# Kernel tuning notes

Hardware: AMD Instinct MI355X
Metric: run time of the kernel (lower is better)

## Reference

```python
import jax, jax.numpy as jnp
import numpy as np

VOCAB, D_IN, D_H, D_OUT, B, S = 32000, 512, 1024, 64, 64, 256


def setup_inputs() -> dict:
    key = jax.random.key(0)
    ks = jax.random.split(key, 8)
    s_in = 1.0 / np.sqrt(D_H)
    return {
        "x": jax.random.randint(ks[0], (B, S), 0, VOCAB),
        "emb": jax.random.normal(ks[1], (VOCAB, D_IN), jnp.float32),
        "w_ih": jax.random.uniform(ks[2], (3 * D_H, D_IN), jnp.float32, -s_in, s_in),
        "w_hh": jax.random.uniform(ks[3], (3 * D_H, D_H), jnp.float32, -s_in, s_in),
        "b_ih": jax.random.uniform(ks[4], (3 * D_H,), jnp.float32, -s_in, s_in),
        "b_hh": jax.random.uniform(ks[5], (3 * D_H,), jnp.float32, -s_in, s_in),
        "fc_w": jax.random.uniform(ks[6], (D_OUT, D_H), jnp.float32, -s_in, s_in),
        "fc_b": jax.random.uniform(ks[7], (D_OUT,), jnp.float32, -s_in, s_in),
    }


def _gru_seq(xe, w_ih, w_hh, b_ih, b_hh):
    # xe: [B, S, D_IN] -> hidden states [B, S, D_H]
    h0 = jnp.zeros((xe.shape[0], D_H), xe.dtype)
    # precompute input projections for all timesteps: [S, B, 3H]
    gi_all = jnp.einsum('bsd,gd->sbg', xe, w_ih) + b_ih

    def step(h, gi):
        gh = h @ w_hh.T + b_hh
        gi_r, gi_z, gi_n = jnp.split(gi, 3, axis=-1)
        gh_r, gh_z, gh_n = jnp.split(gh, 3, axis=-1)
        r = jax.nn.sigmoid(gi_r + gh_r)
        z = jax.nn.sigmoid(gi_z + gh_z)
        n = jnp.tanh(gi_n + r * gh_n)
        h_new = (1.0 - z) * n + z * h
        return h_new, h_new

    _, hs = jax.lax.scan(step, h0, gi_all)  # hs: [S, B, H]
    return jnp.transpose(hs, (1, 0, 2))  # [B, S, H]


def reference(x, emb, w_ih, w_hh, b_ih, b_hh, fc_w, fc_b):
    xe = emb[x]  # [B, S, D_IN]
    outs = _gru_seq(xe, w_ih, w_hh, b_ih, b_hh)  # [B, S, H]
    logits = jnp.einsum('bsh,oh->bso', outs, fc_w) + fc_b
    return jax.nn.log_softmax(logits, axis=2)
```

## Files before the change

kernel.cpp:

```cpp
#include <hip/hip_runtime.h>
#include <stdint.h>
#include <math.h>

typedef short short8 __attribute__((ext_vector_type(8)));
typedef float floatx4 __attribute__((ext_vector_type(4)));

#define MFMA(a, b, c) __builtin_amdgcn_mfma_f32_16x16x32_bf16((a), (b), (c), 0, 0, 0)

#define B_   64
#define S_   256
#define DIN  512
#define DH   1024
#define G3   3072
#define DOUT 64
#define M_   (B_ * S_)
#define NBLK 128
#define FPAD 16
#define NFLAG (S_ * 2 * 128 * FPAD)

#define AGENT_LD_U32(p) __hip_atomic_load((p), __ATOMIC_RELAXED, __HIP_MEMORY_SCOPE_AGENT)
#define AGENT_ST_U32(p, v) __hip_atomic_store((p), (v), __ATOMIC_RELAXED, __HIP_MEMORY_SCOPE_AGENT)

typedef __attribute__((address_space(1))) const void* gas_t;
typedef __attribute__((address_space(3))) void* las_t;

__device__ __forceinline__ unsigned short f2bf(float f) {
    union { float f; uint32_t u; } v; v.f = f;
    uint32_t u = v.u;
    uint32_t r = (u + 0x7fffu + ((u >> 16) & 1u)) >> 16;
    return (unsigned short)r;
}
__device__ __forceinline__ float bf2f(unsigned short s) {
    union { uint32_t u; float f; } v; v.u = ((uint32_t)s) << 16; return v.f;
}
__device__ __forceinline__ short8 ld8(const unsigned short* p) {
    return *reinterpret_cast<const short8*>(p);
}
__device__ __forceinline__ float fast_sigmoid(float x) {
    return 1.f / (1.f + __expf(-x));
}
__device__ __forceinline__ float fast_tanh(float x) {
    return 1.f - 2.f / (__expf(2.f * x) + 1.f);
}

__global__ void cast_bf16_kernel(const float* __restrict__ src,
                                 unsigned short* __restrict__ dst, int n) {
    int i = blockIdx.x * 256 + threadIdx.x;
    if (i < n) dst[i] = f2bf(src[i]);
}

__global__ void init_flags_kernel(unsigned int* flags) {
    int i = blockIdx.x * 256 + threadIdx.x;
    if (i < NFLAG) flags[i] = 0u;
}

__global__ void gather_kernel(const int* __restrict__ x, const float* __restrict__ emb,
                              unsigned short* __restrict__ xe) {
    int g = blockIdx.x * 256 + threadIdx.x;
    int m = g >> 9;
    int k = g & 511;
    int s = m >> 6, b = m & 63;
    int tok = x[b * S_ + s];
    xe[(size_t)m * DIN + k] = f2bf(emb[(size_t)tok * DIN + k]);
}

__global__ __launch_bounds__(256) void gemm_bt_bias(
        const unsigned short* __restrict__ A, const unsigned short* __restrict__ W,
        const float* __restrict__ bias, unsigned short* __restrict__ C,
        int M, int N, int K) {
    __shared__ __align__(16) unsigned short As[128 * 32];
    __shared__ __align__(16) unsigned short Ws[128 * 32];
    int tid = threadIdx.x;
    int lane = tid & 63, wv = tid >> 6;
    int wm = wv >> 1, wn = wv & 1;
    int q = lane >> 4, l15 = lane & 15;
    int bm = blockIdx.x, bn = blockIdx.y;

    floatx4 acc[4][4];
    floatx4 z = {0.f, 0.f, 0.f, 0.f};
    for (int i = 0; i < 4; i++) for (int j = 0; j < 4; j++) acc[i][j] = z;

    const int c0 = wv * 2;
    const int rowc = lane >> 2;
    const int colc = (lane & 3) * 8;
    const unsigned short* gA0 = A + (size_t)(bm * 128 + c0 * 16 + rowc) * K + colc;
    const unsigned short* gA1 = gA0 + (size_t)16 * K;
    const unsigned short* gW0 = W + (size_t)(bn * 128 + c0 * 16 + rowc) * K + colc;
    const unsigned short* gW1 = gW0 + (size_t)16 * K;
    unsigned short* lA0 = &As[c0 * 512];
    unsigned short* lA1 = &As[(c0 + 1) * 512];
    unsigned short* lW0 = &Ws[c0 * 512];
    unsigned short* lW1 = &Ws[(c0 + 1) * 512];

    for (int k0 = 0; k0 < K; k0 += 32) {
        __syncthreads();
        __builtin_amdgcn_global_load_lds((gas_t)(gA0 + k0), (las_t)lA0, 16, 0, 0);
        __builtin_amdgcn_global_load_lds((gas_t)(gA1 + k0), (las_t)lA1, 16, 0, 0);
        __builtin_amdgcn_global_load_lds((gas_t)(gW0 + k0), (las_t)lW0, 16, 0, 0);
        __builtin_amdgcn_global_load_lds((gas_t)(gW1 + k0), (las_t)lW1, 16, 0, 0);
        __syncthreads();
        short8 af[4], wf[4];
        for (int t = 0; t < 4; t++) {
            af[t] = ld8(&As[(wm * 64 + t * 16 + l15) * 32 + q * 8]);
            wf[t] = ld8(&Ws[(wn * 64 + t * 16 + l15) * 32 + q * 8]);
        }
        for (int i = 0; i < 4; i++)
            for (int j = 0; j < 4; j++)
                acc[i][j] = MFMA(af[i], wf[j], acc[i][j]);
    }
    for (int i = 0; i < 4; i++) {
        int row = bm * 128 + wm * 64 + i * 16 + q * 4;
        for (int j = 0; j < 4; j++) {
            int col = bn * 128 + wn * 64 + j * 16 + l15;
            float bv = bias[col];
            for (int r = 0; r < 4; r++)
                C[(size_t)(row + r) * N + col] = f2bf(acc[i][j][r] + bv);
        }
    }
}

__global__ __launch_bounds__(512, 2) void gru_persistent(
        const unsigned short* __restrict__ gi,
        const unsigned short* __restrict__ whh,
        const float* __restrict__ b_hh,
        unsigned short* __restrict__ hs,
        unsigned int* flags) {
    const int tid = threadIdx.x;
    const int lane = tid & 63, wv = tid >> 6;
    const int mt = wv & 1, kh = wv >> 1;
    const int q = lane >> 4, l15 = lane & 15;
    const int jc = blockIdx.x >> 1, mh = blockIdx.x & 1;
    const int j = jc * 16 + l15;
    const int brow0 = mh * 32 + mt * 16;

    __shared__ float red[2][3][2][3][64][4];

    short8 wfrag[3][8];
#pragma unroll
    for (int g = 0; g < 3; g++)
#pragma unroll
        for (int kk = 0; kk < 8; kk++)
            wfrag[g][kk] = ld8(whh + (size_t)(g * 1024 + j) * DH + kh * 256 + kk * 32 + q * 8);

    float bhr = 0.f, bhz = 0.f, bhn = 0.f;
    float hreg[4];
    float gir[4], giz[4], gin[4];
    if (kh == 0) {
        bhr = b_hh[j]; bhz = b_hh[1024 + j]; bhn = b_hh[2048 + j];
#pragma unroll
        for (int r = 0; r < 4; r++) {
            hreg[r] = 0.f;
            int b = brow0 + q * 4 + r;
            gir[r] = bf2f(gi[(size_t)b * G3 + j]);
            giz[r] = bf2f(gi[(size_t)b * G3 + 1024 + j]);
            gin[r] = bf2f(gi[(size_t)b * G3 + 2048 + j]);
        }
    }

    const unsigned int* fbase =
        flags + ((kh * 16 + l15) * 2 + mt) * FPAD + mh * 128 * FPAD;

    for (int s = 0; s < S_; s++) {
        const int pb = s & 1;
        floatx4 zf = {0.f, 0.f, 0.f, 0.f};
        floatx4 acc[3] = {zf, zf, zf};
        if (s > 0) {
            const unsigned int* fp = fbase + (size_t)((s - 1) << 1) * 128 * FPAD;
            while (!__all(AGENT_LD_U32(fp) != 0u)) {
                __builtin_amdgcn_s_sleep(1);
            }
            asm volatile("" ::: "memory");

            const unsigned short* hb =
                hs + ((size_t)((s - 1) * 2 + mh) * 64) * 512 + mt * 256
                   + l15 * 16 + (q & 1) * 8;
            const int jbase = (kh * 16 + (q >> 1)) * 512;
#pragma unroll
            for (int kk = 0; kk < 8; kk++) {
                short8 a = ld8(hb + jbase + kk * 1024);
#pragma unroll
                for (int g = 0; g < 3; g++)
                    acc[g] = MFMA(a, wfrag[g][kk], acc[g]);
            }
        }

        if (kh > 0) {
#pragma unroll
            for (int g = 0; g < 3; g++)
                *reinterpret_cast<floatx4*>(&red[pb][kh - 1][mt][g][lane][0]) = acc[g];
        }
        asm volatile("s_waitcnt lgkmcnt(0)" ::: "memory");
        __builtin_amdgcn_s_barrier();
        asm volatile("" ::: "memory");

        if (kh == 0) {
#pragma unroll
            for (int p = 0; p < 3; p++)
#pragma unroll
                for (int g = 0; g < 3; g++) {
                    floatx4 v = *reinterpret_cast<const floatx4*>(&red[pb][p][mt][g][lane][0]);
                    acc[g] += v;
                }
            uint32_t* ht = (uint32_t*)(hs +
                ((size_t)(s * 2 + mh) * 64 + jc) * 512 + mt * 256);
#pragma unroll
            for (int r = 0; r < 4; r++) {
                float rg = fast_sigmoid(gir[r] + acc[0][r] + bhr);
                float zg = fast_sigmoid(giz[r] + acc[1][r] + bhz);
                float ng = fast_tanh(gin[r] + rg * (acc[2][r] + bhn));
                float h = (1.f - zg) * ng + zg * hreg[r];
                hreg[r] = h;
                float hnb = __shfl_xor(h, 1);
                if ((l15 & 1) == 0) {
                    uint32_t pk = (uint32_t)f2bf(h) | ((uint32_t)f2bf(hnb) << 16);
                    AGENT_ST_U32(&ht[(q * 4 + r) * 8 + (l15 >> 1)], pk);
                }
            }
            if (s + 1 < S_) {
                asm volatile("" ::: "memory");
                asm volatile("s_waitcnt vmcnt(0)" ::: "memory");
                if (lane == 0)
                    AGENT_ST_U32(&flags[(((s << 1) + mh) * 128 + jc * 2 + mt) * FPAD], 1u);
                const unsigned short* gp = gi + (size_t)(s + 1) * B_ * G3;
#pragma unroll
                for (int r = 0; r < 4; r++) {
                    int b = brow0 + q * 4 + r;
                    gir[r] = bf2f(gp[(size_t)b * G3 + j]);
                    giz[r] = bf2f(gp[(size_t)b * G3 + 1024 + j]);
                    gin[r] = bf2f(gp[(size_t)b * G3 + 2048 + j]);
                }
            }
        }
    }
}

__global__ __launch_bounds__(256) void fc_logsoftmax(
        const unsigned short* __restrict__ hs,
        const unsigned short* __restrict__ fcw,
        const float* __restrict__ fcb,
        float* __restrict__ out) {
    int tid = threadIdx.x;
    int lane = tid & 63, mt = tid >> 6;
    int q = lane >> 4, l15 = lane & 15;
    int s = blockIdx.x;

    floatx4 acc[4];
    floatx4 z = {0.f, 0.f, 0.f, 0.f};
    for (int nt = 0; nt < 4; nt++) acc[nt] = z;

    int b = mt * 16 + l15;
    int mh = b >> 5, mtb = (b >> 4) & 1, r16 = b & 15;
    const unsigned short* Ab =
        hs + ((size_t)(s * 2 + mh) * 64) * 512 + mtb * 256
           + r16 * 16 + (q & 1) * 8;
    const int jq = (q >> 1) * 512;
    const unsigned short* Wp = fcw + (size_t)l15 * DH + q * 8;
    for (int k0 = 0; k0 < DH; k0 += 32) {
        short8 a = ld8(Ab + (k0 >> 4) * 512 + jq);
        for (int nt = 0; nt < 4; nt++)
            acc[nt] = MFMA(a, ld8(Wp + (size_t)nt * 16 * DH + k0), acc[nt]);
    }

    float bv[4];
    for (int nt = 0; nt < 4; nt++) bv[nt] = fcb[nt * 16 + l15];

    for (int r = 0; r < 4; r++) {
        float v[4];
        for (int nt = 0; nt < 4; nt++) v[nt] = acc[nt][r] + bv[nt];
        float m = fmaxf(fmaxf(v[0], v[1]), fmaxf(v[2], v[3]));
        for (int off = 1; off < 16; off <<= 1) m = fmaxf(m, __shfl_xor(m, off));
        float se = __expf(v[0] - m) + __expf(v[1] - m) + __expf(v[2] - m) + __expf(v[3] - m);
        for (int off = 1; off < 16; off <<= 1) se += __shfl_xor(se, off);
        float L = logf(se);
        int brow = mt * 16 + q * 4 + r;
        float* op = out + (size_t)(brow * S_ + s) * DOUT;
        for (int nt = 0; nt < 4; nt++) op[nt * 16 + l15] = v[nt] - m - L;
    }
}

extern "C" void kernel_launch(void* const* d_in, const int* in_sizes, int n_in,
                              void* d_out, int out_size, void* d_ws, size_t ws_size,
                              hipStream_t stream) {
    const int*   x    = (const int*)d_in[0];
    const float* emb  = (const float*)d_in[1];
    const float* w_ih = (const float*)d_in[2];
    const float* w_hh = (const float*)d_in[3];
    const float* b_ih = (const float*)d_in[4];
    const float* b_hh = (const float*)d_in[5];
    const float* fc_w = (const float*)d_in[6];
    const float* fc_b = (const float*)d_in[7];
    float* out = (float*)d_out;

    char* p = (char*)d_ws;
    unsigned int*   flags = (unsigned int*)p;   p += (size_t)NFLAG * 4;
    unsigned short* xe    = (unsigned short*)p; p += (size_t)M_ * DIN * 2;
    unsigned short* gi    = (unsigned short*)p; p += (size_t)M_ * G3 * 2;
    unsigned short* wih_b = (unsigned short*)p; p += (size_t)G3 * DIN * 2;
    unsigned short* whh_b = (unsigned short*)p; p += (size_t)G3 * DH * 2;
    unsigned short* fcw_b = (unsigned short*)p; p += (size_t)DOUT * DH * 2;
    unsigned short* hs    = (unsigned short*)p; p += (size_t)M_ * DH * 2;

    init_flags_kernel<<<(NFLAG + 255) / 256, 256, 0, stream>>>(flags);
    cast_bf16_kernel<<<(G3 * DIN + 255) / 256, 256, 0, stream>>>(w_ih, wih_b, G3 * DIN);
    cast_bf16_kernel<<<(G3 * DH + 255) / 256, 256, 0, stream>>>(w_hh, whh_b, G3 * DH);
    cast_bf16_kernel<<<(DOUT * DH + 255) / 256, 256, 0, stream>>>(fc_w, fcw_b, DOUT * DH);
    gather_kernel<<<(M_ * DIN) / 256, 256, 0, stream>>>(x, emb, xe);

    gemm_bt_bias<<<dim3(M_ / 128, G3 / 128), 256, 0, stream>>>(
        xe, wih_b, b_ih, gi, M_, G3, DIN);

    gru_persistent<<<NBLK, 512, 0, stream>>>(gi, whh_b, b_hh, hs, flags);

    fc_logsoftmax<<<S_, 256, 0, stream>>>(hs, fcw_b, fc_b, out);
}
```

Before: 1.163 ms.

## Use poison-value validation of hidden state to overlap loads with flag wait

Pre-fills the hidden-state buffer with a NaN-like poison pattern and has consumers speculatively load the previous step's h before the flag is set, then validate the loaded words against the poison and reload with cache-bypassing loads until all are valid. The producer no longer waits for its h stores to complete before raising the flag, which shortens the critical path of each recurrent step. In exchange it adds a full poison-fill pass over hs, per-step validation compares, and relies on a real bf16 pair never matching the poison pattern. It also relies on the visibility ordering of relaxed atomics without the vmcnt wait.

```diff
diff --git a/kernel.cpp b/kernel.cpp
--- a/kernel.cpp
+++ b/kernel.cpp
@@ -4,6 +4,7 @@
 
 typedef short short8 __attribute__((ext_vector_type(8)));
 typedef float floatx4 __attribute__((ext_vector_type(4)));
+typedef uint32_t uint4v __attribute__((ext_vector_type(4)));
 
 #define MFMA(a, b, c) __builtin_amdgcn_mfma_f32_16x16x32_bf16((a), (b), (c), 0, 0, 0)
 
@@ -18,6 +19,8 @@
 #define FPAD 16
 #define NFLAG (S_ * 2 * 128 * FPAD)
 
+#define POISON 0xFFC0FFC0u
+
 #define AGENT_LD_U32(p) __hip_atomic_load((p), __ATOMIC_RELAXED, __HIP_MEMORY_SCOPE_AGENT)
 #define AGENT_ST_U32(p, v) __hip_atomic_store((p), (v), __ATOMIC_RELAXED, __HIP_MEMORY_SCOPE_AGENT)
 
@@ -43,6 +46,27 @@
     return 1.f - 2.f / (__expf(2.f * x) + 1.f);
 }
 
+__device__ __forceinline__ void reload_tile8(
+        const unsigned short* p0, const unsigned short* p1,
+        const unsigned short* p2, const unsigned short* p3,
+        short8& a0, short8& a1, short8& a2, short8& a3,
+        short8& a4, short8& a5, short8& a6, short8& a7) {
+    asm volatile(
+        "global_load_dwordx4 %0, %8, off sc0 sc1\n\t"
+        "global_load_dwordx4 %1, %8, off offset:2048 sc0 sc1\n\t"
+        "global_load_dwordx4 %2, %9, off sc0 sc1\n\t"
+        "global_load_dwordx4 %3, %9, off offset:2048 sc0 sc1\n\t"
+        "global_load_dwordx4 %4, %10, off sc0 sc1\n\t"
+        "global_load_dwordx4 %5, %10, off offset:2048 sc0 sc1\n\t"
+        "global_load_dwordx4 %6, %11, off sc0 sc1\n\t"
+        "global_load_dwordx4 %7, %11, off offset:2048 sc0 sc1\n\t"
+        "s_waitcnt vmcnt(0)"
+        : "=&v"(a0), "=&v"(a1), "=&v"(a2), "=&v"(a3),
+          "=&v"(a4), "=&v"(a5), "=&v"(a6), "=&v"(a7)
+        : "v"(p0), "v"(p1), "v"(p2), "v"(p3)
+        : "memory");
+}
+
 __global__ void cast_bf16_kernel(const float* __restrict__ src,
                                  unsigned short* __restrict__ dst, int n) {
     int i = blockIdx.x * 256 + threadIdx.x;
@@ -52,6 +76,13 @@
 __global__ void init_flags_kernel(unsigned int* flags) {
     int i = blockIdx.x * 256 + threadIdx.x;
     if (i < NFLAG) flags[i] = 0u;
+}
+
+__global__ void poison_hs_kernel(uint4v* hs4) {
+    size_t i = (size_t)blockIdx.x * 256 + threadIdx.x;
+    size_t n = (size_t)M_ * DH / 8;
+    uint4v pv = {POISON, POISON, POISON, POISON};
+    if (i < n) hs4[i] = pv;
 }
 
 __global__ void gather_kernel(const int* __restrict__ x, const float* __restrict__ emb,
@@ -160,28 +191,48 @@
     const unsigned int* fbase =
         flags + ((kh * 16 + l15) * 2 + mt) * FPAD + mh * 128 * FPAD;
 
+    union Frag { short8 v[8]; uint32_t w[32]; };
+
     for (int s = 0; s < S_; s++) {
         const int pb = s & 1;
         floatx4 zf = {0.f, 0.f, 0.f, 0.f};
         floatx4 acc[3] = {zf, zf, zf};
         if (s > 0) {
             const unsigned int* fp = fbase + (size_t)((s - 1) << 1) * 128 * FPAD;
-            while (!__all(AGENT_LD_U32(fp) != 0u)) {
+            const unsigned short* hbs =
+                hs + ((size_t)((s - 1) * 2 + mh) * 64) * 512 + mt * 256
+                   + l15 * 16 + (q & 1) * 8 + (size_t)(kh * 16 + (q >> 1)) * 512;
+            Frag f;
+            bool have = false;
+            if (!__all(AGENT_LD_U32(fp) != 0u)) {
+#pragma unroll
+                for (int kk = 0; kk < 8; kk++) f.v[kk] = ld8(hbs + kk * 1024);
+                have = true;
+                asm volatile("" ::: "memory");
+                while (!__all(AGENT_LD_U32(fp) != 0u)) {
+                    __builtin_amdgcn_s_sleep(1);
+                }
+            }
+            asm volatile("" ::: "memory");
+            if (!have) {
+#pragma unroll
+                for (int kk = 0; kk < 8; kk++) f.v[kk] = ld8(hbs + kk * 1024);
+            }
+            for (;;) {
+                uint32_t ok = 1u;
+#pragma unroll
+                for (int t = 0; t < 32; t++) ok &= (uint32_t)(f.w[t] != POISON);
+                if (__all(ok != 0u)) break;
                 __builtin_amdgcn_s_sleep(1);
-            }
-            asm volatile("" ::: "memory");
-
-            const unsigned short* hb =
-                hs + ((size_t)((s - 1) * 2 + mh) * 64) * 512 + mt * 256
-                   + l15 * 16 + (q & 1) * 8;
-            const int jbase = (kh * 16 + (q >> 1)) * 512;
-#pragma unroll
-            for (int kk = 0; kk < 8; kk++) {
-                short8 a = ld8(hb + jbase + kk * 1024);
+                reload_tile8(hbs, hbs + 2048, hbs + 4096, hbs + 6144,
+                             f.v[0], f.v[1], f.v[2], f.v[3],
+                             f.v[4], f.v[5], f.v[6], f.v[7]);
+            }
+#pragma unroll
+            for (int kk = 0; kk < 8; kk++)
 #pragma unroll
                 for (int g = 0; g < 3; g++)
-                    acc[g] = MFMA(a, wfrag[g][kk], acc[g]);
-            }
+                    acc[g] = MFMA(f.v[kk], wfrag[g][kk], acc[g]);
         }
 
         if (kh > 0) {
@@ -218,7 +269,6 @@
             }
             if (s + 1 < S_) {
                 asm volatile("" ::: "memory");
-                asm volatile("s_waitcnt vmcnt(0)" ::: "memory");
                 if (lane == 0)
                     AGENT_ST_U32(&flags[(((s << 1) + mh) * 128 + jc * 2 + mt) * FPAD], 1u);
                 const unsigned short* gp = gi + (size_t)(s + 1) * B_ * G3;
@@ -301,6 +351,7 @@
     unsigned short* hs    = (unsigned short*)p; p += (size_t)M_ * DH * 2;
 
     init_flags_kernel<<<(NFLAG + 255) / 256, 256, 0, stream>>>(flags);
+    poison_hs_kernel<<<(M_ * DH / 8 + 255) / 256, 256, 0, stream>>>((uint4v*)hs);
     cast_bf16_kernel<<<(G3 * DIN + 255) / 256, 256, 0, stream>>>(w_ih, wih_b, G3 * DIN);
     cast_bf16_kernel<<<(G3 * DH + 255) / 256, 256, 0, stream>>>(w_hh, whh_b, G3 * DH);
     cast_bf16_kernel<<<(DOUT * DH + 255) / 256, 256, 0, stream>>>(fc_w, fcw_b, DOUT * DH);
```

Result: slower. 1.767 ms (+51.9%).
